# Kernel tuning notes

Measured on AMD Instinct MI355X. Metric: run time of the kernel, lower is better.

## Reference

```python
import jax, jax.numpy as jnp
import numpy as np

IMAGE_H, IMAGE_W = 256, 704
Z, Y, X = 128, 8, 128
BOUNDS = (-50.0, 50.0, -5.0, 5.0, -50.0, 50.0)
CENTROID = (0.0, 1.0, 0.0)
EPS_MEAN = 1e-6
EPS_DEPTH = 1e-4


def _compose_rt(R, t):
    M = jnp.zeros(R.shape[:-2] + (4, 4), R.dtype)
    M = M.at[..., :3, :3].set(R)
    M = M.at[..., :3, 3].set(t)
    M = M.at[..., 3, 3].set(1.0)
    return M


def _safe_inverse(M):
    R = M[..., :3, :3]
    t = M[..., :3, 3]
    Rt = jnp.swapaxes(R, -1, -2)
    return _compose_rt(Rt, -jnp.einsum('...ij,...j->...i', Rt, t))


def _apply_4x4(M, xyz):
    # M: (...,4,4), xyz: (...,N,3) -> (...,N,3)
    return jnp.einsum('...ij,...nj->...ni', M[..., :3, :3], xyz) + M[..., None, :3, 3]


def _xyz_camA():
    # Mem2Ref of gridcloud3d: x_ref = x_mem*vox + MIN + vox/2 (bounds shifted by centroid)
    xmin = BOUNDS[0] + CENTROID[0]; xmax = BOUNDS[1] + CENTROID[0]
    ymin = BOUNDS[2] + CENTROID[1]; ymax = BOUNDS[3] + CENTROID[1]
    zmin = BOUNDS[4] + CENTROID[2]; zmax = BOUNDS[5] + CENTROID[2]
    vx = (xmax - xmin) / X; vy = (ymax - ymin) / Y; vz = (zmax - zmin) / Z
    zz, yy, xx = jnp.meshgrid(jnp.arange(Z, dtype=jnp.float32),
                              jnp.arange(Y, dtype=jnp.float32),
                              jnp.arange(X, dtype=jnp.float32), indexing='ij')
    x = xx * vx + xmin + vx / 2.0
    y = yy * vy + ymin + vy / 2.0
    z = zz * vz + zmin + vz / 2.0
    return jnp.stack([x, y, z], -1).reshape(Z * Y * X, 3)  # mem order (Z,Y,X)


def _bilinear_sample(img, px, py):
    # img: (C,H,W); px,py: (N,) pixel coords; zeros padding (grid_sample align_corners=False)
    C, H, W = img.shape
    x0 = jnp.floor(px); y0 = jnp.floor(py)
    dx = px - x0; dy = py - y0
    x0i = x0.astype(jnp.int32); y0i = y0.astype(jnp.int32)
    flat = img.reshape(C, H * W)

    def gather(yi, xi, w):
        inb = (xi >= 0) & (xi < W) & (yi >= 0) & (yi < H)
        idx = jnp.clip(yi, 0, H - 1) * W + jnp.clip(xi, 0, W - 1)
        return flat[:, idx] * (w * inb.astype(img.dtype))

    return (gather(y0i, x0i, (1 - dx) * (1 - dy))
            + gather(y0i, x0i + 1, dx * (1 - dy))
            + gather(y0i + 1, x0i, (1 - dx) * dy)
            + gather(y0i + 1, x0i + 1, dx * dy))  # (C,N)


def _forward(cam_feat, camera2ego, cam_intrinsic, conv_w):
    B, S, C, Hf, Wf = cam_feat.shape
    # velo_T_cams = merge_rt(camera2ego R, t); cam0_T_camXs = inv(velo_T_cams[:,0]) @ velo_T_cams
    velo_T_cams = _compose_rt(camera2ego[..., :3, :3], camera2ego[..., :3, 3])
    cam0_T_velo = _safe_inverse(velo_T_cams[:, 0])
    cam0_T_camXs = jnp.einsum('bij,bsjk->bsik', cam0_T_velo, velo_T_cams)
    camXs_T_cam0 = _safe_inverse(cam0_T_camXs)
    # scale_intrinsics with sy = Hf/H*0.284, sx = Wf/W*0.44
    sy = Hf / float(IMAGE_H) * 0.284
    sx = Wf / float(IMAGE_W) * 0.44
    fx = cam_intrinsic[..., 0, 0] * sx
    fy = cam_intrinsic[..., 1, 1] * sy
    cx = cam_intrinsic[..., 0, 2] * sx
    cy = cam_intrinsic[..., 1, 2] * sy
    K = jnp.zeros((B, S, 4, 4), cam_feat.dtype)
    K = K.at[..., 0, 0].set(fx).at[..., 1, 1].set(fy)
    K = K.at[..., 0, 2].set(cx).at[..., 1, 2].set(cy)
    K = K.at[..., 2, 2].set(1.0).at[..., 3, 3].set(1.0)
    pixB_T_cam0 = jnp.einsum('bsij,bsjk->bsik', K, camXs_T_cam0)

    xyz = _xyz_camA()  # (N,3), N = Z*Y*X
    xyz_camB = _apply_4x4(camXs_T_cam0, xyz[None, None])  # (B,S,N,3)
    z_cam = xyz_camB[..., 2]
    xyz_pix = _apply_4x4(pixB_T_cam0, xyz[None, None])
    depth = jnp.maximum(xyz_pix[..., 2], EPS_DEPTH)
    x_pix = xyz_pix[..., 0] / depth
    y_pix = xyz_pix[..., 1] / depth
    valid = ((x_pix > -0.5) & (x_pix < Wf - 0.5)
             & (y_pix > -0.5) & (y_pix < Hf - 0.5)
             & (z_cam > 0.0)).astype(cam_feat.dtype)
    # normalize_grid2d (clamp [-2,2]) then grid_sample align_corners=False unnormalize
    gx = jnp.clip(2.0 * x_pix / (Wf - 1) - 1.0, -2.0, 2.0)
    gy = jnp.clip(2.0 * y_pix / (Hf - 1) - 1.0, -2.0, 2.0)
    px = ((gx + 1.0) * Wf - 1.0) / 2.0
    py = ((gy + 1.0) * Hf - 1.0) / 2.0

    feats = cam_feat.reshape(B * S, C, Hf, Wf)
    vals = jax.vmap(_bilinear_sample)(feats, px.reshape(B * S, -1), py.reshape(B * S, -1))
    vals = vals.reshape(B, S, C, -1) * valid[:, :, None, :]  # (B,S,C,N)
    mask = (jnp.abs(vals) > 0).astype(vals.dtype)
    feat_mem = jnp.sum(vals * mask, axis=1) / (EPS_MEAN + jnp.sum(mask, axis=1))  # (B,C,N)
    feat_mem = feat_mem.reshape(B, C, Z, Y, X)

    # BEV compress: permute(0,1,3,2,4) -> (B, C*Y, Z, X), conv3x3 (no bias), InstanceNorm2d, GELU
    feat_bev = jnp.transpose(feat_mem, (0, 1, 3, 2, 4)).reshape(B, C * Y, Z, X)
    out = jax.lax.conv_general_dilated(feat_bev, conv_w, (1, 1), ((1, 1), (1, 1)),
                                       dimension_numbers=('NCHW', 'OIHW', 'NCHW'))
    mu = jnp.mean(out, axis=(2, 3), keepdims=True)
    var = jnp.var(out, axis=(2, 3), keepdims=True)
    out = (out - mu) / jnp.sqrt(var + 1e-5)
    return jax.nn.gelu(out, approximate=False)


def setup_inputs() -> dict:
    key = jax.random.key(0)
    k1, k2, k3 = jax.random.split(key, 3)
    B, S, C, Hf, Wf = 1, 6, 128, 32, 88
    cam_feat = jax.random.normal(k1, (B, S, C, Hf, Wf), jnp.float32)
    # rigid camera2ego: yaw rotations about the y axis + small translations
    yaws = jnp.arange(S, dtype=jnp.float32) * (2.0 * jnp.pi / S)
    c, s = jnp.cos(yaws), jnp.sin(yaws)
    zr, on = jnp.zeros_like(c), jnp.ones_like(c)
    R = jnp.stack([jnp.stack([c, zr, s], -1),
                   jnp.stack([zr, on, zr], -1),
                   jnp.stack([-s, zr, c], -1)], -2)  # (S,3,3)
    t = jax.random.normal(k2, (S, 3), jnp.float32) * 0.5
    cam2ego = jnp.zeros((B, S, 4, 4), jnp.float32)
    cam2ego = cam2ego.at[0, :, :3, :3].set(R).at[0, :, :3, 3].set(t).at[0, :, 3, 3].set(1.0)
    K = jnp.zeros((B, S, 4, 4), jnp.float32)
    K = K.at[..., 0, 0].set(600.0).at[..., 1, 1].set(600.0)
    K = K.at[..., 0, 2].set(352.0).at[..., 1, 2].set(128.0)
    K = K.at[..., 2, 2].set(1.0).at[..., 3, 3].set(1.0)
    conv_w = jax.random.normal(k3, (128, 128 * Y, 3, 3), jnp.float32) / np.sqrt(128 * Y * 9.0).astype(np.float32)
    return {"cam_feat": cam_feat, "camera2ego": cam2ego, "cam_intrinsic": K, "conv_w": conv_w}


def reference(cam_feat, camera2ego, cam_intrinsic, conv_w):
    return _forward(cam_feat, camera2ego, cam_intrinsic, conv_w)
```

## Files before the change

### kernel.cpp

```cpp
#include <hip/hip_runtime.h>
#include <hip/hip_bf16.h>
#include <math.h>

#define HF 32
#define WF 88
#define NCAM 6
#define CC 128
#define ZD 128
#define YD 8
#define XD 128

using f32x4  = __attribute__((ext_vector_type(4))) float;
using bf16x8 = __attribute__((ext_vector_type(8))) short;
using h2     = __attribute__((ext_vector_type(2))) _Float16;

#if defined(__has_builtin)
#if __has_builtin(__builtin_amdgcn_fdot2)
#define HAVE_FDOT2 1
#endif
#endif
__device__ __forceinline__ float fdot2f(h2 a, h2 b, float c) {
#ifdef HAVE_FDOT2
  return __builtin_amdgcn_fdot2(a, b, c, false);
#else
  return c + (float)a[0] * (float)b[0] + (float)a[1] * (float)b[1];
#endif
}

#define OFF_P    0ull
#define OFF_W    512ull
#define OFF_CAMT (OFF_W + 2359296ull)
#define OFF_F    (OFF_CAMT + 8650752ull)
#define OFF_CONV (OFF_F + 34611200ull)

__global__ __launch_bounds__(256) void k_pre(const float* __restrict__ feat,
                                             const float* __restrict__ conv_w,
                                             const float* __restrict__ cam2ego,
                                             const float* __restrict__ intr,
                                             unsigned* __restrict__ camT2,
                                             __hip_bfloat16* __restrict__ wp,
                                             float* __restrict__ P) {
  __shared__ float tile[128 * 89];
  const int b = blockIdx.x;
  const int t = threadIdx.x;
  if (b < 192) {
    const int s = b >> 5;
    const int hrow = b & 31;
    for (int idx = t; idx < 128 * 88; idx += 256) {
      const int c = idx / 88;
      const int w = idx - c * 88;
      tile[c * 89 + w] = feat[((size_t)(s * CC + c) * HF + hrow) * WF + w];
    }
    __syncthreads();
    unsigned* dst = camT2 + (size_t)(s * 32 + hrow) * 87 * 128;
    for (int idx = t; idx < 87 * 128; idx += 256) {
      const int px = idx >> 7;
      const int c = idx & 127;
      union { _Float16 h[2]; unsigned u; } pr;
      pr.h[0] = (_Float16)tile[c * 89 + px];
      pr.h[1] = (_Float16)tile[c * 89 + px + 1];
      dst[px * 128 + c] = pr.u;
    }
  } else if (b < 704) {
    const int tt = (b - 192) * 256 + t;
    float v[9];
    #pragma unroll
    for (int d = 0; d < 9; d++) v[d] = conv_w[(size_t)tt * 9 + d];
    #pragma unroll
    for (int d = 0; d < 9; d++) wp[(size_t)d * 131072 + tt] = __float2bfloat16(v[d]);
  } else {
    const int s = t;
    if (s >= NCAM) return;
    const float* M0 = cam2ego;
    const float* Ms = cam2ego + s * 16;
    float Rb[9], tb[3];
    for (int i = 0; i < 3; i++)
      for (int j = 0; j < 3; j++) {
        float v = 0.f;
        for (int k = 0; k < 3; k++) v += Ms[k * 4 + i] * M0[k * 4 + j];
        Rb[i * 3 + j] = v;
      }
    for (int i = 0; i < 3; i++) {
      float v = 0.f;
      for (int k = 0; k < 3; k++) v += Ms[k * 4 + i] * (M0[k * 4 + 3] - Ms[k * 4 + 3]);
      tb[i] = v;
    }
    const float* Ks = intr + s * 16;
    const float sx = (float)WF / 704.0f * 0.44f;
    const float sy = (float)HF / 256.0f * 0.284f;
    const float fx = Ks[0] * sx, fy = Ks[5] * sy;
    const float cx = Ks[2] * sx, cy = Ks[6] * sy;
    float* p = P + s * 12;
    for (int j = 0; j < 3; j++) p[j]     = fx * Rb[j]     + cx * Rb[6 + j];
    p[3]  = fx * tb[0] + cx * tb[2];
    for (int j = 0; j < 3; j++) p[4 + j] = fy * Rb[3 + j] + cy * Rb[6 + j];
    p[7]  = fy * tb[1] + cy * tb[2];
    for (int j = 0; j < 3; j++) p[8 + j] = Rb[6 + j];
    p[11] = tb[2];
  }
}

struct Rec { int offA; int offB; unsigned wA; unsigned wB; };

__global__ __launch_bounds__(256) void k2_sample(const unsigned* __restrict__ camT2,
                                                 const float* __restrict__ P,
                                                 __hip_bfloat16* __restrict__ F) {
  const int bz = blockIdx.x / 65;
  const int bxp = blockIdx.x % 65;
  const int t = threadIdx.x;
  const int sub = t >> 7;
  const int u = t & 127;
  const int bx = bxp * 2 + sub;
  const int zi = bz - 1, xi = bx - 1;
  const int cq = (u & 31) << 2;
  const int yq = u >> 5;
  __hip_bfloat16* Fb = F + ((size_t)bz * 130 + bx) * 1024;
  const bool inplay = !(zi < 0 || zi >= ZD || xi < 0 || xi >= XD);

  __shared__ Rec recs[2][48];
  __shared__ unsigned ymask[2][8];
  const int lane = t & 63;
  const int wv = t >> 6;
  bool vflag = false;
  if ((wv == 0 || wv == 2) && lane < 48 && inplay) {
    const int y = lane / 6, s = lane - y * 6;
    const float* pp = P + s * 12;
    const float vx = 100.0f / 128.0f;
    const float xw = xi * vx - 50.0f + vx * 0.5f;
    const float zw = zi * vx - 50.0f + vx * 0.5f;
    const float yw = y * 1.25f - 4.0f + 0.625f;
    const float zc = pp[8] * xw + pp[9] * yw + pp[10] * zw + pp[11];
    const float xp = pp[0] * xw + pp[1] * yw + pp[2] * zw + pp[3];
    const float yp = pp[4] * xw + pp[5] * yw + pp[6] * zw + pp[7];
    const float dep = fmaxf(zc, 1e-4f);
    const float pxf = xp / dep, pyf = yp / dep;
    const bool valid = (pxf > -0.5f && pxf < (float)WF - 0.5f &&
                        pyf > -0.5f && pyf < (float)HF - 0.5f && zc > 0.0f);
    const float px = pxf * ((float)WF / (float)(WF - 1)) - 0.5f;
    const float py = pyf * ((float)HF / (float)(HF - 1)) - 0.5f;
    const float fx0 = floorf(px), fy0 = floorf(py);
    const float ddx = px - fx0, ddy = py - fy0;
    const int x0i = (int)fx0, y0i = (int)fy0;
    const float vf = valid ? 1.0f : 0.0f;
    const float wxl = (1.0f - ddx) * vf, wxr = ddx * vf;
    int pxi; float sl, sr;
    if (x0i >= 0 && x0i <= 86)      { pxi = x0i; sl = wxl; sr = wxr; }
    else if (x0i == -1)             { pxi = 0;   sl = wxr; sr = 0.f; }
    else if (x0i == 87)             { pxi = 86;  sl = 0.f; sr = wxl; }
    else                            { pxi = 0;   sl = 0.f; sr = 0.f; }
    const float fA = ((unsigned)y0i < (unsigned)HF) ? (1.0f - ddy) : 0.0f;
    const float fB = ((unsigned)(y0i + 1) < (unsigned)HF) ? ddy : 0.0f;
    const int rowA = min(max(y0i, 0), HF - 1);
    const int rowB = min(max(y0i + 1, 0), HF - 1);
    Rec r;
    r.offA = ((s * HF + rowA) * 87 + pxi) * 128;
    r.offB = ((s * HF + rowB) * 87 + pxi) * 128;
    union { _Float16 h[2]; unsigned u; } wa, wb;
    wa.h[0] = (_Float16)(sl * fA); wa.h[1] = (_Float16)(sr * fA);
    wb.h[0] = (_Float16)(sl * fB); wb.h[1] = (_Float16)(sr * fB);
    r.wA = wa.u; r.wB = wb.u;
    recs[sub][lane] = r;
    vflag = ((sl + sr) * (fA + fB)) > 0.0f;
  }
  if (wv == 0 || wv == 2) {
    unsigned long long m = __ballot(vflag);
    if (lane < 8) ymask[wv >> 1][lane] = (unsigned)((m >> (6 * lane)) & 63ull);
  }
  __syncthreads();

  if (!inplay) {
    #pragma unroll
    for (int j = 0; j < 4; j++)
      *reinterpret_cast<unsigned*>(Fb + (cq + j) * 8 + yq * 2) = 0u;
    return;
  }

  float num[2][4] = {{0.f, 0.f, 0.f, 0.f}, {0.f, 0.f, 0.f, 0.f}};
  int cnt[2] = {0, 0};
  #pragma unroll
  for (int yi = 0; yi < 2; yi++) {
    const int y = yq * 2 + yi;
    unsigned ms = ymask[sub][y];
    while (ms) {
      const int s = __builtin_ctz(ms);
      ms &= ms - 1;
      const Rec r = recs[sub][y * 6 + s];
      const uint4 a4 = *reinterpret_cast<const uint4*>(&camT2[r.offA + cq]);
      const uint4 b4 = *reinterpret_cast<const uint4*>(&camT2[r.offB + cq]);
      const h2 wa = __builtin_bit_cast(h2, r.wA);
      const h2 wb = __builtin_bit_cast(h2, r.wB);
      num[yi][0] = fdot2f(__builtin_bit_cast(h2, a4.x), wa, num[yi][0]);
      num[yi][1] = fdot2f(__builtin_bit_cast(h2, a4.y), wa, num[yi][1]);
      num[yi][2] = fdot2f(__builtin_bit_cast(h2, a4.z), wa, num[yi][2]);
      num[yi][3] = fdot2f(__builtin_bit_cast(h2, a4.w), wa, num[yi][3]);
      num[yi][0] = fdot2f(__builtin_bit_cast(h2, b4.x), wb, num[yi][0]);
      num[yi][1] = fdot2f(__builtin_bit_cast(h2, b4.y), wb, num[yi][1]);
      num[yi][2] = fdot2f(__builtin_bit_cast(h2, b4.z), wb, num[yi][2]);
      num[yi][3] = fdot2f(__builtin_bit_cast(h2, b4.w), wb, num[yi][3]);
      cnt[yi]++;
    }
  }
  const float inv0 = 1.0f / (1e-6f + (float)cnt[0]);
  const float inv1 = 1.0f / (1e-6f + (float)cnt[1]);
  #pragma unroll
  for (int j = 0; j < 4; j++) {
    __hip_bfloat16 o[2];
    o[0] = __float2bfloat16(num[0][j] * inv0);
    o[1] = __float2bfloat16(num[1][j] * inv1);
    *reinterpret_cast<unsigned*>(Fb + (cq + j) * 8 + yq * 2) =
        *reinterpret_cast<const unsigned*>(o);
  }
}

__device__ __forceinline__ void load_lds16(const void* g, void* l) {
  __builtin_amdgcn_global_load_lds(
      (const __attribute__((address_space(1))) unsigned int*)g,
      (__attribute__((address_space(3))) unsigned int*)l, 16, 0, 0);
}

#define K3_NT 72

__global__ __launch_bounds__(512) void k3_gemm(const __hip_bfloat16* __restrict__ F,
                                               const __hip_bfloat16* __restrict__ Wp,
                                               float* __restrict__ out0,
                                               float* __restrict__ out1) {
  const int orig = (blockIdx.x & 7) * 32 + (blockIdx.x >> 3);
  const int z = orig & 127;
  const int h = orig >> 7;
  const int ciH = h << 9;
  const int tid = threadIdx.x;
  const int w = tid >> 6;
  const int l = tid & 63;
  const int kk = w >> 2;
  const int wq = w & 3;
  const int wm = wq >> 1;
  const int wn = wq & 1;
  __shared__ __hip_bfloat16 lds[4][16384];

  f32x4 acc[4][4];
  #pragma unroll
  for (int m = 0; m < 4; m++)
    #pragma unroll
    for (int n = 0; n < 4; n++)
      acc[m][n] = (f32x4){0.f, 0.f, 0.f, 0.f};

  auto stage_A = [&](int kt) {
    const int buf = kt & 3;
    const int d = kt >> 3;
    const int dz = d / 3, dx = d - dz * 3;
    const int ci0 = ciH + ((kt & 7) << 6);
    const int zbase = (z + dz) * 130 + dx;
    #pragma unroll
    for (int i = 0; i < 2; i++) {
      const int n = w * 128 + i * 64 + l;
      const int row = n >> 3;
      const int q = (n & 7) ^ (row & 7);
      const __hip_bfloat16* src = F + ((size_t)(zbase + row) << 10) + ci0 + (q << 3);
      load_lds16(src, &lds[buf][(w * 128 + i * 64) * 8]);
    }
  };
  auto stage_B = [&](int kt) {
    const int buf = kt & 3;
    const int d = kt >> 3;
    const int ci0 = ciH + ((kt & 7) << 6);
    #pragma unroll
    for (int i = 0; i < 2; i++) {
      const int n = w * 128 + i * 64 + l;
      const int co = n >> 3;
      const int q = (n & 7) ^ (co & 7);
      const __hip_bfloat16* src = Wp + ((size_t)d << 17) + ((size_t)co << 10) + ci0 + (q << 3);
      load_lds16(src, &lds[buf][8192 + (w * 128 + i * 64) * 8]);
    }
  };

  const int r16 = l & 15;
  const int hi = l >> 4;
  const int cslot = kk * 4 + hi;

  auto step = [&](int t, bool doStage, int wcode) {
    const int buf = t & 3;
    bf16x8 a[4], b[4];
    #pragma unroll
    for (int m = 0; m < 4; m++) {
      const int r = wm * 64 + m * 16 + r16;
      const int slot = cslot ^ (r & 7);
      a[m] = *reinterpret_cast<const bf16x8*>(&lds[buf][r * 64 + slot * 8]);
    }
    #pragma unroll
    for (int n = 0; n < 2; n++) {
      const int co = wn * 64 + n * 16 + r16;
      const int slot = cslot ^ (co & 7);
      b[n] = *reinterpret_cast<const bf16x8*>(&lds[buf][8192 + co * 64 + slot * 8]);
    }
    if (doStage) stage_A(t + 3);
    __builtin_amdgcn_s_barrier();
    __builtin_amdgcn_s_setprio(1);
    #pragma unroll
    for (int m = 0; m < 4; m++) {
      acc[m][0] = __builtin_amdgcn_mfma_f32_16x16x32_bf16(a[m], b[0], acc[m][0], 0, 0, 0);
      acc[m][1] = __builtin_amdgcn_mfma_f32_16x16x32_bf16(a[m], b[1], acc[m][1], 0, 0, 0);
    }
    __builtin_amdgcn_s_setprio(0);
    __builtin_amdgcn_s_barrier();
    #pragma unroll
    for (int n = 2; n < 4; n++) {
      const int co = wn * 64 + n * 16 + r16;
      const int slot = cslot ^ (co & 7);
      b[n] = *reinterpret_cast<const bf16x8*>(&lds[buf][8192 + co * 64 + slot * 8]);
    }
    if (doStage) stage_B(t + 3);
    __builtin_amdgcn_s_barrier();
    __builtin_amdgcn_s_setprio(1);
    #pragma unroll
    for (int m = 0; m < 4; m++) {
      acc[m][2] = __builtin_amdgcn_mfma_f32_16x16x32_bf16(a[m], b[2], acc[m][2], 0, 0, 0);
      acc[m][3] = __builtin_amdgcn_mfma_f32_16x16x32_bf16(a[m], b[3], acc[m][3], 0, 0, 0);
    }
    __builtin_amdgcn_s_setprio(0);
    if (wcode == 8)      asm volatile("s_waitcnt vmcnt(8)" ::: "memory");
    else if (wcode == 4) asm volatile("s_waitcnt vmcnt(4)" ::: "memory");
    else if (wcode == 0) asm volatile("s_waitcnt vmcnt(0)" ::: "memory");
    __builtin_amdgcn_s_barrier();
  };

  stage_A(0); stage_B(0); stage_A(1); stage_B(1); stage_A(2); stage_B(2);
  asm volatile("s_waitcnt vmcnt(8)" ::: "memory");
  __builtin_amdgcn_s_barrier();

  for (int t = 0; t < K3_NT - 3; ++t) step(t, true, 8);
  step(K3_NT - 3, false, 4);
  step(K3_NT - 2, false, 0);
  step(K3_NT - 1, false, -1);

  float* red = reinterpret_cast<float*>(&lds[0][0]);
  if (kk == 1) {
    float* dst = red + wq * 4096;
    #pragma unroll
    for (int m = 0; m < 4; m++)
      #pragma unroll
      for (int n = 0; n < 4; n++)
        *reinterpret_cast<f32x4*>(&dst[(m * 4 + n) * 256 + l * 4]) = acc[m][n];
  }
  __syncthreads();
  if (kk == 0) {
    const float* srcr = red + wq * 4096;
    float* outP = h ? out1 : out0;
    #pragma unroll
    for (int m = 0; m < 4; m++) {
      const int xr = wm * 64 + m * 16 + hi * 4;
      #pragma unroll
      for (int n = 0; n < 4; n++) {
        f32x4 o = *reinterpret_cast<const f32x4*>(&srcr[(m * 4 + n) * 256 + l * 4]);
        f32x4 r = acc[m][n] + o;
        const int co = wn * 64 + n * 16 + r16;
        *reinterpret_cast<f32x4*>(&outP[((size_t)co << 14) + (z << 7) + xr]) = r;
      }
    }
  }
}

__device__ __forceinline__ float gelu_exact(float x) {
  return 0.5f * x * (1.0f + erff(x * 0.70710678118654752440f));
}

__global__ __launch_bounds__(1024) void k4_ln(const float* __restrict__ c0,
                                              const float* __restrict__ c1,
                                              float* __restrict__ outp) {
  const int co = blockIdx.x;
  const int t = threadIdx.x;
  const float4* p0 = reinterpret_cast<const float4*>(c0 + ((size_t)co << 14));
  const float4* p1 = reinterpret_cast<const float4*>(c1 + ((size_t)co << 14));
  float4 v[4];
  float s = 0.f, s2 = 0.f;
  #pragma unroll
  for (int i = 0; i < 4; i++) {
    float4 a = p0[t + (i << 10)];
    float4 b = p1[t + (i << 10)];
    float4 r;
    r.x = a.x + b.x; r.y = a.y + b.y; r.z = a.z + b.z; r.w = a.w + b.w;
    v[i] = r;
    s  += r.x + r.y + r.z + r.w;
    s2 += r.x * r.x + r.y * r.y + r.z * r.z + r.w * r.w;
  }
  #pragma unroll
  for (int off = 32; off > 0; off >>= 1) {
    s  += __shfl_down(s, off);
    s2 += __shfl_down(s2, off);
  }
  __shared__ float red[32];
  __shared__ float mb[2];
  const int wv = t >> 6, ln = t & 63;
  if (ln == 0) { red[wv] = s; red[wv + 16] = s2; }
  __syncthreads();
  if (t == 0) {
    float S = 0.f, S2 = 0.f;
    #pragma unroll
    for (int i = 0; i < 16; i++) { S += red[i]; S2 += red[i + 16]; }
    float mu = S * (1.0f / 16384.0f);
    float var = S2 * (1.0f / 16384.0f) - mu * mu;
    mb[0] = mu;
    mb[1] = 1.0f / sqrtf(var + 1e-5f);
  }
  __syncthreads();
  const float mu = mb[0], inv = mb[1];
  float4* op = reinterpret_cast<float4*>(outp + ((size_t)co << 14));
  #pragma unroll
  for (int i = 0; i < 4; i++) {
    float4 x = v[i];
    float4 r;
    r.x = gelu_exact((x.x - mu) * inv);
    r.y = gelu_exact((x.y - mu) * inv);
    r.z = gelu_exact((x.z - mu) * inv);
    r.w = gelu_exact((x.w - mu) * inv);
    op[t + (i << 10)] = r;
  }
}

extern "C" void kernel_launch(void* const* d_in, const int* in_sizes, int n_in,
                              void* d_out, int out_size, void* d_ws, size_t ws_size,
                              hipStream_t stream) {
  const float* cam_feat = (const float*)d_in[0];
  const float* cam2ego  = (const float*)d_in[1];
  const float* intr     = (const float*)d_in[2];
  const float* conv_w   = (const float*)d_in[3];
  float* out = (float*)d_out;
  char* ws = (char*)d_ws;

  float*          P     = (float*)(ws + OFF_P);
  __hip_bfloat16* Wp    = (__hip_bfloat16*)(ws + OFF_W);
  unsigned*       camT2 = (unsigned*)(ws + OFF_CAMT);
  __hip_bfloat16* F     = (__hip_bfloat16*)(ws + OFF_F);
  float*          conv0 = (float*)(ws + OFF_CONV);
  float*          conv1 = (float*)(ws + OFF_CAMT);

  hipLaunchKernelGGL(k_pre, dim3(705), dim3(256), 0, stream,
                     cam_feat, conv_w, cam2ego, intr, camT2, Wp, P);
  hipLaunchKernelGGL(k2_sample, dim3(130 * 65), dim3(256), 0, stream, camT2, P, F);
  hipLaunchKernelGGL(k3_gemm, dim3(256), dim3(512), 0, stream, F, Wp, conv0, conv1);
  hipLaunchKernelGGL(k4_ln, dim3(128), dim3(1024), 0, stream, conv0, conv1, out);
}
```

Measured before the change: 100.7 us.

## Map one wavefront per BEV cell in sampling kernel, use shuffles instead of LDS

The sampling kernel now assigns each 64-lane wavefront to one (z,x) cell. Each lane covers two channel pairs across all 8 y levels, instead of splitting a cell across 128 threads by channel quad and y pair. Per-camera projection records are broadcast with wave shuffles and a ballot, which removes the shared-memory record table and the block barrier. Output is written as two 16-byte stores per lane. The trade-off is narrower 8-byte gathers per lane and a serial loop over all 8 y levels per wave, which may reduce memory-level parallelism.

```diff
diff --git a/kernel.cpp b/kernel.cpp
--- a/kernel.cpp
+++ b/kernel.cpp
@@ -100,30 +100,29 @@
   }
 }
 
-struct Rec { int offA; int offB; unsigned wA; unsigned wB; };
-
 __global__ __launch_bounds__(256) void k2_sample(const unsigned* __restrict__ camT2,
                                                  const float* __restrict__ P,
                                                  __hip_bfloat16* __restrict__ F) {
-  const int bz = blockIdx.x / 65;
-  const int bxp = blockIdx.x % 65;
-  const int t = threadIdx.x;
-  const int sub = t >> 7;
-  const int u = t & 127;
-  const int bx = bxp * 2 + sub;
+  const int wv = threadIdx.x >> 6;
+  const int l  = threadIdx.x & 63;
+  const int cell = blockIdx.x * 4 + wv;
+  const int bz = cell / 130;
+  const int bx = cell - bz * 130;
   const int zi = bz - 1, xi = bx - 1;
-  const int cq = (u & 31) << 2;
-  const int yq = u >> 5;
-  __hip_bfloat16* Fb = F + ((size_t)bz * 130 + bx) * 1024;
-  const bool inplay = !(zi < 0 || zi >= ZD || xi < 0 || xi >= XD);
-
-  __shared__ Rec recs[2][48];
-  __shared__ unsigned ymask[2][8];
-  const int lane = t & 63;
-  const int wv = t >> 6;
+  __hip_bfloat16* Fb = F + (size_t)cell * 1024;
+
+  if (zi < 0 || zi >= ZD || xi < 0 || xi >= XD) {
+    const uint4 z4 = {0u, 0u, 0u, 0u};
+    *reinterpret_cast<uint4*>(Fb + (2 * l) * 8)     = z4;
+    *reinterpret_cast<uint4*>(Fb + (2 * l + 1) * 8) = z4;
+    return;
+  }
+
+  int offA = 0, offB = 0;
+  unsigned pwA = 0, pwB = 0;
   bool vflag = false;
-  if ((wv == 0 || wv == 2) && lane < 48 && inplay) {
-    const int y = lane / 6, s = lane - y * 6;
+  if (l < 48) {
+    const int y = l / 6, s = l - y * 6;
     const float* pp = P + s * 12;
     const float vx = 100.0f / 128.0f;
     const float xw = xi * vx - 50.0f + vx * 0.5f;
@@ -152,64 +151,54 @@
     const float fB = ((unsigned)(y0i + 1) < (unsigned)HF) ? ddy : 0.0f;
     const int rowA = min(max(y0i, 0), HF - 1);
     const int rowB = min(max(y0i + 1, 0), HF - 1);
-    Rec r;
-    r.offA = ((s * HF + rowA) * 87 + pxi) * 128;
-    r.offB = ((s * HF + rowB) * 87 + pxi) * 128;
+    offA = ((s * HF + rowA) * 87 + pxi) * 128;
+    offB = ((s * HF + rowB) * 87 + pxi) * 128;
     union { _Float16 h[2]; unsigned u; } wa, wb;
     wa.h[0] = (_Float16)(sl * fA); wa.h[1] = (_Float16)(sr * fA);
     wb.h[0] = (_Float16)(sl * fB); wb.h[1] = (_Float16)(sr * fB);
-    r.wA = wa.u; r.wB = wb.u;
-    recs[sub][lane] = r;
+    pwA = wa.u; pwB = wb.u;
     vflag = ((sl + sr) * (fA + fB)) > 0.0f;
   }
-  if (wv == 0 || wv == 2) {
-    unsigned long long m = __ballot(vflag);
-    if (lane < 8) ymask[wv >> 1][lane] = (unsigned)((m >> (6 * lane)) & 63ull);
-  }
-  __syncthreads();
-
-  if (!inplay) {
-    #pragma unroll
-    for (int j = 0; j < 4; j++)
-      *reinterpret_cast<unsigned*>(Fb + (cq + j) * 8 + yq * 2) = 0u;
-    return;
-  }
-
-  float num[2][4] = {{0.f, 0.f, 0.f, 0.f}, {0.f, 0.f, 0.f, 0.f}};
-  int cnt[2] = {0, 0};
-  #pragma unroll
-  for (int yi = 0; yi < 2; yi++) {
-    const int y = yq * 2 + yi;
-    unsigned ms = ymask[sub][y];
+  const unsigned long long m = __ballot(vflag);
+
+  float accA[8], accB[8];
+  #pragma unroll
+  for (int y = 0; y < 8; y++) { accA[y] = 0.f; accB[y] = 0.f; }
+
+  #pragma unroll
+  for (int y = 0; y < 8; y++) {
+    unsigned ms = (unsigned)((m >> (6 * y)) & 63ull);
+    const int c = __popc(ms);
     while (ms) {
       const int s = __builtin_ctz(ms);
       ms &= ms - 1;
-      const Rec r = recs[sub][y * 6 + s];
-      const uint4 a4 = *reinterpret_cast<const uint4*>(&camT2[r.offA + cq]);
-      const uint4 b4 = *reinterpret_cast<const uint4*>(&camT2[r.offB + cq]);
-      const h2 wa = __builtin_bit_cast(h2, r.wA);
-      const h2 wb = __builtin_bit_cast(h2, r.wB);
-      num[yi][0] = fdot2f(__builtin_bit_cast(h2, a4.x), wa, num[yi][0]);
-      num[yi][1] = fdot2f(__builtin_bit_cast(h2, a4.y), wa, num[yi][1]);
-      num[yi][2] = fdot2f(__builtin_bit_cast(h2, a4.z), wa, num[yi][2]);
-      num[yi][3] = fdot2f(__builtin_bit_cast(h2, a4.w), wa, num[yi][3]);
-      num[yi][0] = fdot2f(__builtin_bit_cast(h2, b4.x), wb, num[yi][0]);
-      num[yi][1] = fdot2f(__builtin_bit_cast(h2, b4.y), wb, num[yi][1]);
-      num[yi][2] = fdot2f(__builtin_bit_cast(h2, b4.z), wb, num[yi][2]);
-      num[yi][3] = fdot2f(__builtin_bit_cast(h2, b4.w), wb, num[yi][3]);
-      cnt[yi]++;
-    }
-  }
-  const float inv0 = 1.0f / (1e-6f + (float)cnt[0]);
-  const float inv1 = 1.0f / (1e-6f + (float)cnt[1]);
-  #pragma unroll
-  for (int j = 0; j < 4; j++) {
-    __hip_bfloat16 o[2];
-    o[0] = __float2bfloat16(num[0][j] * inv0);
-    o[1] = __float2bfloat16(num[1][j] * inv1);
-    *reinterpret_cast<unsigned*>(Fb + (cq + j) * 8 + yq * 2) =
-        *reinterpret_cast<const unsigned*>(o);
-  }
+      const int src = y * 6 + s;
+      const int oA = __shfl(offA, src);
+      const int oB = __shfl(offB, src);
+      const unsigned uwA = (unsigned)__shfl((int)pwA, src);
+      const unsigned uwB = (unsigned)__shfl((int)pwB, src);
+      const uint2 av = *reinterpret_cast<const uint2*>(camT2 + oA + 2 * l);
+      const uint2 bv = *reinterpret_cast<const uint2*>(camT2 + oB + 2 * l);
+      const h2 wa = __builtin_bit_cast(h2, uwA);
+      const h2 wb = __builtin_bit_cast(h2, uwB);
+      accA[y] = fdot2f(__builtin_bit_cast(h2, av.x), wa, accA[y]);
+      accB[y] = fdot2f(__builtin_bit_cast(h2, av.y), wa, accB[y]);
+      accA[y] = fdot2f(__builtin_bit_cast(h2, bv.x), wb, accA[y]);
+      accB[y] = fdot2f(__builtin_bit_cast(h2, bv.y), wb, accB[y]);
+    }
+    const float inv = 1.0f / (1e-6f + (float)c);
+    accA[y] *= inv;
+    accB[y] *= inv;
+  }
+
+  union { __hip_bfloat16 h[8]; uint4 u; } pA, pB;
+  #pragma unroll
+  for (int y = 0; y < 8; y++) {
+    pA.h[y] = __float2bfloat16(accA[y]);
+    pB.h[y] = __float2bfloat16(accB[y]);
+  }
+  *reinterpret_cast<uint4*>(Fb + (2 * l) * 8)     = pA.u;
+  *reinterpret_cast<uint4*>(Fb + (2 * l + 1) * 8) = pB.u;
 }
 
 __device__ __forceinline__ void load_lds16(const void* g, void* l) {
@@ -435,7 +424,7 @@
 
   hipLaunchKernelGGL(k_pre, dim3(705), dim3(256), 0, stream,
                      cam_feat, conv_w, cam2ego, intr, camT2, Wp, P);
-  hipLaunchKernelGGL(k2_sample, dim3(130 * 65), dim3(256), 0, stream, camT2, P, F);
+  hipLaunchKernelGGL(k2_sample, dim3(4225), dim3(256), 0, stream, camT2, P, F);
   hipLaunchKernelGGL(k3_gemm, dim3(256), dim3(512), 0, stream, F, Wp, conv0, conv1);
   hipLaunchKernelGGL(k4_ln, dim3(128), dim3(1024), 0, stream, conv0, conv1, out);
 }
```

After: 95.69 us (median of 2 runs). 1.05x faster.
